# Optimization experiments

Measured on AMD Instinct MI355X. Metric: run time of the kernel, lower is better.

## Reference

```python
import jax, jax.numpy as jnp
import numpy as np

CUTOFF = 4.0
RBF_N = 32          # distance_embedding_size == D_rbf
F_DIM = 128         # hidden_size
N_ATOMS = 20000
N_PROBES = 100000
N_EDGES = 262144
LN_EPS = 1e-5


def setup_inputs() -> dict:
    key = jax.random.key(0)
    ks = jax.random.split(key, 20)
    s = 0.02
    inp = {
        "diff_pi": jax.random.normal(ks[0], (N_EDGES, 3), jnp.float32),
        "S_JK": jax.random.normal(ks[1], (N_ATOMS, F_DIM), jnp.float32),
        "V_JK": jax.random.normal(ks[2], (N_ATOMS, 3, F_DIM), jnp.float32),
        "atom_idx": jax.random.randint(ks[3], (N_EDGES,), 0, N_ATOMS),
        "probe_idx": jax.random.randint(ks[4], (N_EDGES,), 0, N_PROBES),
        "num_probes": N_PROBES,
        # state branch params
        "w_s1": jax.random.normal(ks[5], (3 * F_DIM, F_DIM), jnp.float32) * s,
        "b_s1": jnp.zeros((F_DIM,), jnp.float32),
        "g_ln": jnp.ones((F_DIM,), jnp.float32),
        "b_ln": jnp.zeros((F_DIM,), jnp.float32),
        "w_s2": jax.random.normal(ks[6], (F_DIM, F_DIM), jnp.float32) * s,
        "b_s2": jnp.zeros((F_DIM,), jnp.float32),
        # filter branch params
        "w_f1": jax.random.normal(ks[7], (RBF_N, F_DIM), jnp.float32) * s,
        "b_f1": jnp.zeros((F_DIM,), jnp.float32),
        "w_f2": jax.random.normal(ks[8], (F_DIM, F_DIM), jnp.float32) * s,
        "b_f2": jnp.zeros((F_DIM,), jnp.float32),
        # output head params
        "w_o1": jax.random.normal(ks[9], (F_DIM, F_DIM // 2), jnp.float32) * s,
        "b_o1": jnp.zeros((F_DIM // 2,), jnp.float32),
        "w_o2": jax.random.normal(ks[10], (F_DIM // 2, 1), jnp.float32) * s,
        "b_o2": jnp.zeros((1,), jnp.float32),
        "final_bias": jnp.array([-6.1], jnp.float32),
    }
    return inp


def reference(diff_pi, S_JK, V_JK, atom_idx, probe_idx, num_probes,
              w_s1, b_s1, g_ln, b_ln, w_s2, b_s2,
              w_f1, b_f1, w_f2, b_f2,
              w_o1, b_o1, w_o2, b_o2, final_bias):
    silu = jax.nn.silu
    # edge distances
    sq = (diff_pi ** 2).sum(-1)                       # [E]
    dist = jnp.sqrt(sq)                               # [E] exact distance
    dist_safe = jnp.sqrt(sq + 1e-8)[:, None]          # [E,1]
    r_hat = diff_pi / dist_safe                       # [E,3]

    # sinc RBF expansion: sin(n*pi*d/cutoff)/d, n=1..RBF_N
    n = jnp.arange(1, RBF_N + 1, dtype=diff_pi.dtype) # [D]
    e_pi = jnp.sin(dist[:, None] * n * (jnp.pi / CUTOFF)) / dist[:, None]  # [E,D]

    # gather atom features to edges
    n_i = jnp.sqrt((V_JK ** 2).sum(1) + 1e-8)         # [N,F]
    n_e = n_i[atom_idx]                               # [E,F]
    V_e = V_JK[atom_idx]                              # [E,3,F]
    q_pi = (V_e * r_hat[:, :, None]).sum(1)           # [E,F]
    S_e = S_JK[atom_idx]                              # [E,F]

    # state branch: Linear -> LayerNorm -> SiLU -> Linear
    h = jnp.concatenate([S_e, n_e, q_pi], axis=-1)    # [E,3F]
    u = h @ w_s1 + b_s1                               # [E,F]
    mu = u.mean(-1, keepdims=True)
    var = ((u - mu) ** 2).mean(-1, keepdims=True)
    u_norm = (u - mu) / jnp.sqrt(var + LN_EPS) * g_ln + b_ln
    state = silu(u_norm) @ w_s2 + b_s2                # [E,F]

    # filter branch (no normalization -> absolute distance scale)
    W = silu(e_pi @ w_f1 + b_f1) @ w_f2 + b_f2        # [E,F]

    # fuse + output head
    m = (silu((W * state) @ w_o1 + b_o1) @ w_o2 + b_o2)[:, 0]  # [E]

    x = dist / CUTOFF
    env = 1.0 - 21.0 * x ** 5 + 35.0 * x ** 6 - 15.0 * x ** 7
    env = jnp.where(dist < CUTOFF, env, jnp.zeros_like(env))
    m_w = m * env

    # scatter-add to probes
    rho = jax.ops.segment_sum(m_w, probe_idx, num_segments=num_probes)
    return rho + final_bias[0]
```

## Files before the change

kernel.cpp:

```cpp
#include <hip/hip_runtime.h>

#define EPB     64
#define E_TOTAL 262144
#define NPROBE  100000
#define N_ATOMS 20000

#define ASTR   136
#define A2_O   0
#define F1_O   8704
#define EPI_O  17408
#define DIST_O 19968
#define LDS_SH 20096

#define WS1_O  0
#define WS2_O  49152
#define WF1_O  65536
#define WF2_O  69632
#define WO1_O  86016
#define WT_TOT 94208
#define PQ_O   WT_TOT

typedef __attribute__((ext_vector_type(8))) short          short8;
typedef __attribute__((ext_vector_type(8))) unsigned short ushort8;
typedef __attribute__((ext_vector_type(4))) float          floatx4;

#define MFMA16(a, b, c) __builtin_amdgcn_mfma_f32_16x16x32_bf16((a), (b), (c), 0, 0, 0)

__device__ __forceinline__ short f2bf(float x) {
    unsigned u = __builtin_bit_cast(unsigned, x);
    u = (u + 0x7FFFu + ((u >> 16) & 1u)) >> 16;
    return (short)(unsigned short)u;
}
__device__ __forceinline__ unsigned pk2(float lo, float hi) {
    return __builtin_amdgcn_perm(__builtin_bit_cast(unsigned, hi),
                                 __builtin_bit_cast(unsigned, lo), 0x07060302u);
}
__device__ __forceinline__ float bf2f(unsigned short u) {
    return __builtin_bit_cast(float, ((unsigned)u) << 16);
}
__device__ __forceinline__ float silu_f(float x) {
    return x * __builtin_amdgcn_rcpf(1.0f + __expf(-x));
}

struct F8 { float v[8]; };
__device__ __forceinline__ F8 ld8(const float* __restrict__ p) {
    F8 r;
    const float4 a = *(const float4*)p;
    const float4 b = *(const float4*)(p + 4);
    r.v[0] = a.x; r.v[1] = a.y; r.v[2] = a.z; r.v[3] = a.w;
    r.v[4] = b.x; r.v[5] = b.y; r.v[6] = b.z; r.v[7] = b.w;
    return r;
}

__global__ void cfr_prep_w(const float* __restrict__ w_s1, const float* __restrict__ w_s2,
                           const float* __restrict__ w_f1, const float* __restrict__ w_f2,
                           const float* __restrict__ w_o1,
                           const float* __restrict__ fb, float* __restrict__ out,
                           unsigned short* __restrict__ wt) {
    int i = blockIdx.x * 256 + threadIdx.x;
    if (i < NPROBE) out[i] = fb[0];
    if (i < WT_TOT) {
        float v;
        if (i < WS2_O)      { int n = i / 384, k = i - n * 384;          v = w_s1[k * 128 + n]; }
        else if (i < WF1_O) { int j = i - WS2_O, n = j >> 7, k = j & 127; v = w_s2[k * 128 + n]; }
        else if (i < WF2_O) { int j = i - WF1_O, n = j >> 5, k = j & 31;  v = w_f1[k * 128 + n]; }
        else if (i < WO1_O) { int j = i - WF2_O, n = j >> 7, k = j & 127; v = w_f2[k * 128 + n]; }
        else                { int j = i - WO1_O, n = j >> 7, k = j & 127; v = w_o1[k * 64 + n]; }
        wt[i] = (unsigned short)f2bf(v);
    }
}

__global__ __launch_bounds__(256, 2) void cfr_prep_pq(
    const float* __restrict__ S, const float* __restrict__ V,
    const float* __restrict__ b_s1,
    const unsigned short* __restrict__ wt, unsigned short* __restrict__ pq)
{
    __shared__ __align__(16) unsigned short bufH[64 * 256];
    __shared__ __align__(16) unsigned short bufV[192 * 128];

    const int t    = threadIdx.x;
    const int a0   = blockIdx.x * 64;
    const int wave = t >> 6;
    const int lane = t & 63;
    const int q    = lane >> 4;
    const int c16  = lane & 15;

#pragma unroll
    for (int it = 0; it < 4; ++it) {
        int idx = it * 256 + t;
        int al = idx >> 4, f8 = (idx & 15) * 8;
        int a = a0 + al;
        ushort8 sS, sN, s0, s1, s2;
        if (a < N_ATOMS) {
            F8 s  = ld8(S + a * 128 + f8);
            F8 v0 = ld8(V + a * 384 + f8);
            F8 v1 = ld8(V + a * 384 + 128 + f8);
            F8 v2 = ld8(V + a * 384 + 256 + f8);
#pragma unroll
            for (int j = 0; j < 8; ++j) {
                sS[j] = (unsigned short)f2bf(s.v[j]);
                sN[j] = (unsigned short)f2bf(sqrtf(v0.v[j]*v0.v[j] + v1.v[j]*v1.v[j] + v2.v[j]*v2.v[j] + 1e-8f));
                s0[j] = (unsigned short)f2bf(v0.v[j]);
                s1[j] = (unsigned short)f2bf(v1.v[j]);
                s2[j] = (unsigned short)f2bf(v2.v[j]);
            }
        } else {
#pragma unroll
            for (int j = 0; j < 8; ++j) { sS[j]=0; sN[j]=0; s0[j]=0; s1[j]=0; s2[j]=0; }
        }
        const unsigned swH = (unsigned)((al & 7) << 4);
        char* hrow  = (char*)bufH + al * 512;
        char* vbase = (char*)bufV;
        *(ushort8*)(hrow + ((f8 * 2) ^ swH))         = sS;
        *(ushort8*)(hrow + ((256 + f8 * 2) ^ swH))   = sN;
        *(ushort8*)(vbase + al * 256         + ((f8 * 2) ^ swH)) = s0;
        *(ushort8*)(vbase + (64 + al) * 256  + ((f8 * 2) ^ swH)) = s1;
        *(ushort8*)(vbase + (128 + al) * 256 + ((f8 * 2) ^ swH)) = s2;
    }
    __syncthreads();

    const floatx4 zero4 = {0.f, 0.f, 0.f, 0.f};
    const unsigned swr = (unsigned)((c16 & 7) << 4);
    float bs1c[2];
#pragma unroll
    for (int ni = 0; ni < 2; ++ni) bs1c[ni] = b_s1[wave * 32 + ni * 16 + c16];

    {
        floatx4 pacc[4][2];
#pragma unroll
        for (int mi = 0; mi < 4; ++mi) { pacc[mi][0] = zero4; pacc[mi][1] = zero4; }
#pragma unroll
        for (int kk = 0; kk < 8; ++kk) {
            short8 bfr[2], af[4];
#pragma unroll
            for (int ni = 0; ni < 2; ++ni) {
                int n = wave * 32 + ni * 16 + c16;
                bfr[ni] = *(const short8*)&wt[WS1_O + n * 384 + kk * 32 + q * 8];
            }
#pragma unroll
            for (int mi = 0; mi < 4; ++mi) {
                int row = mi * 16 + c16;
                af[mi] = *(const short8*)((const char*)bufH + row * 512 + ((unsigned)(kk * 64 + q * 16) ^ swr));
            }
#pragma unroll
            for (int mi = 0; mi < 4; ++mi)
#pragma unroll
                for (int ni = 0; ni < 2; ++ni)
                    pacc[mi][ni] = MFMA16(af[mi], bfr[ni], pacc[mi][ni]);
        }
#pragma unroll
        for (int mi = 0; mi < 4; ++mi)
#pragma unroll
            for (int r = 0; r < 4; ++r) {
                int a = a0 + mi * 16 + q * 4 + r;
                if (a < N_ATOMS)
#pragma unroll
                    for (int ni = 0; ni < 2; ++ni) {
                        int col = wave * 32 + ni * 16 + c16;
                        pq[a * 512 + col] = (unsigned short)f2bf(pacc[mi][ni][r] + bs1c[ni]);
                    }
            }
    }

    short8 bq[4][2];
#pragma unroll
    for (int kk = 0; kk < 4; ++kk)
#pragma unroll
        for (int ni = 0; ni < 2; ++ni) {
            int n = wave * 32 + ni * 16 + c16;
            bq[kk][ni] = *(const short8*)&wt[WS1_O + n * 384 + 256 + kk * 32 + q * 8];
        }
#pragma unroll
    for (int d = 0; d < 3; ++d) {
        floatx4 qacc[4][2];
#pragma unroll
        for (int mi = 0; mi < 4; ++mi) { qacc[mi][0] = zero4; qacc[mi][1] = zero4; }
#pragma unroll
        for (int kk = 0; kk < 4; ++kk) {
            short8 af[4];
#pragma unroll
            for (int mi = 0; mi < 4; ++mi) {
                int row = d * 64 + mi * 16 + c16;
                af[mi] = *(const short8*)((const char*)bufV + row * 256 + ((unsigned)(kk * 64 + q * 16) ^ swr));
            }
#pragma unroll
            for (int mi = 0; mi < 4; ++mi)
#pragma unroll
                for (int ni = 0; ni < 2; ++ni)
                    qacc[mi][ni] = MFMA16(af[mi], bq[kk][ni], qacc[mi][ni]);
        }
#pragma unroll
        for (int mi = 0; mi < 4; ++mi)
#pragma unroll
            for (int r = 0; r < 4; ++r) {
                int a = a0 + mi * 16 + q * 4 + r;
                if (a < N_ATOMS)
#pragma unroll
                    for (int ni = 0; ni < 2; ++ni) {
                        int col = wave * 32 + ni * 16 + c16;
                        pq[a * 512 + (1 + d) * 128 + col] = (unsigned short)f2bf(qacc[mi][ni][r]);
                    }
            }
    }
}

__global__ __launch_bounds__(256, 2) void cfr_main(
    const float* __restrict__ diff,
    const int* __restrict__ atom_idx, const int* __restrict__ probe_idx,
    const unsigned short* __restrict__ wt, const unsigned short* __restrict__ pq,
    const float* __restrict__ g_ln, const float* __restrict__ b_ln,
    const float* __restrict__ b_s2, const float* __restrict__ b_f1,
    const float* __restrict__ b_f2, const float* __restrict__ b_o1,
    const float* __restrict__ w_o2, const float* __restrict__ b_o2,
    float* __restrict__ out)
{
    __shared__ __align__(16) unsigned short LDSu[LDS_SH];
    float* mpart = (float*)&LDSu[EPI_O];
    float* distL = (float*)&LDSu[DIST_O];

    const int t    = threadIdx.x;
    const int e0   = blockIdx.x * EPB;
    const int wave = t >> 6;
    const int lane = t & 63;
    const int q    = lane >> 4;
    const int c16  = lane & 15;
    const floatx4 zero4 = {0.f, 0.f, 0.f, 0.f};

    short8 wbe[2];
    short8 wb2[4][2], wbw[4][2];
    short8 wbo[4];
    float  bf1c[2], bs2c[2], bf2c[2];
#pragma unroll
    for (int ni = 0; ni < 2; ++ni) {
        const int n = wave * 32 + ni * 16 + c16;
        wbe[ni] = *(const short8*)&wt[WF1_O + n * 32 + q * 8];
#pragma unroll
        for (int kk = 0; kk < 4; ++kk) {
            wb2[kk][ni] = *(const short8*)&wt[WS2_O + n * 128 + kk * 32 + q * 8];
            wbw[kk][ni] = *(const short8*)&wt[WF2_O + n * 128 + kk * 32 + q * 8];
        }
        bf1c[ni] = b_f1[n]; bs2c[ni] = b_s2[n]; bf2c[ni] = b_f2[n];
    }
    const int n2 = wave * 16 + c16;
#pragma unroll
    for (int kk = 0; kk < 4; ++kk)
        wbo[kk] = *(const short8*)&wt[WO1_O + n2 * 128 + kk * 32 + q * 8];
    const float bo1c = b_o1[n2], wo2c = w_o2[n2];

    {
        const int el = t >> 2;
        const int cc = t & 3;
        const int c0 = cc * 32;
        const int eg = e0 + el;
        const int a  = atom_idx[eg];
        float dx = diff[eg * 3 + 0], dy = diff[eg * 3 + 1], dz = diff[eg * 3 + 2];
        float sq   = dx * dx + dy * dy + dz * dz;
        float dist = sqrtf(sq);
        float rinv = rsqrtf(sq + 1e-8f);
        float rx = dx * rinv, ry = dy * rinv, rz = dz * rinv;
        if (cc == 0) distL[el] = dist;

        const ushort8* pqr = (const ushort8*)(pq + a * 512 + c0);
        float u[32];
#pragma unroll
        for (int g = 0; g < 4; ++g) {
            ushort8 v = pqr[g];
#pragma unroll
            for (int j = 0; j < 8; ++j) u[g * 8 + j] = bf2f(v[j]);
        }
#pragma unroll
        for (int g = 0; g < 4; ++g) {
            ushort8 v = pqr[16 + g];
#pragma unroll
            for (int j = 0; j < 8; ++j) u[g * 8 + j] = fmaf(bf2f(v[j]), rx, u[g * 8 + j]);
        }
#pragma unroll
        for (int g = 0; g < 4; ++g) {
            ushort8 v = pqr[32 + g];
#pragma unroll
            for (int j = 0; j < 8; ++j) u[g * 8 + j] = fmaf(bf2f(v[j]), ry, u[g * 8 + j]);
        }
#pragma unroll
        for (int g = 0; g < 4; ++g) {
            ushort8 v = pqr[48 + g];
#pragma unroll
            for (int j = 0; j < 8; ++j) u[g * 8 + j] = fmaf(bf2f(v[j]), rz, u[g * 8 + j]);
        }
        float s = 0.f, s2 = 0.f;
#pragma unroll
        for (int j = 0; j < 32; ++j) { s += u[j]; s2 = fmaf(u[j], u[j], s2); }
        s  += __shfl_xor(s, 1);  s  += __shfl_xor(s, 2);
        s2 += __shfl_xor(s2, 1); s2 += __shfl_xor(s2, 2);
        float mu = s * (1.f / 128.f);
        float rstd = rsqrtf(s2 * (1.f / 128.f) - mu * mu + 1e-5f);
        const float4* gp = (const float4*)(g_ln + c0);
        const float4* bp = (const float4*)(b_ln + c0);
        unsigned pko[16];
#pragma unroll
        for (int g4 = 0; g4 < 8; ++g4) {
            float4 gg = gp[g4], bb = bp[g4];
            float y0 = silu_f((u[g4 * 4 + 0] - mu) * rstd * gg.x + bb.x);
            float y1 = silu_f((u[g4 * 4 + 1] - mu) * rstd * gg.y + bb.y);
            float y2 = silu_f((u[g4 * 4 + 2] - mu) * rstd * gg.z + bb.z);
            float y3 = silu_f((u[g4 * 4 + 3] - mu) * rstd * gg.w + bb.w);
            pko[g4 * 2 + 0] = pk2(y0, y1);
            pko[g4 * 2 + 1] = pk2(y2, y3);
        }
        uint4* dst = (uint4*)&LDSu[A2_O + el * ASTR + c0];
        dst[0] = make_uint4(pko[0], pko[1], pko[2], pko[3]);
        dst[1] = make_uint4(pko[4], pko[5], pko[6], pko[7]);
        dst[2] = make_uint4(pko[8], pko[9], pko[10], pko[11]);
        dst[3] = make_uint4(pko[12], pko[13], pko[14], pko[15]);
        float inv = __builtin_amdgcn_rcpf(dist);
        float d8  = dist * 0.125f;
        float sv[8];
#pragma unroll
        for (int j = 0; j < 8; ++j) {
            float nf = (float)(cc * 8 + j + 1);
            sv[j] = __builtin_amdgcn_sinf(d8 * nf) * inv;
        }
        *(uint4*)&LDSu[EPI_O + el * 40 + cc * 8] =
            make_uint4(pk2(sv[0], sv[1]), pk2(sv[2], sv[3]), pk2(sv[4], sv[5]), pk2(sv[6], sv[7]));
    }
    __syncthreads();

    {
        short8 ae[4];
#pragma unroll
        for (int mi = 0; mi < 4; ++mi)
            ae[mi] = *(const short8*)&LDSu[EPI_O + (mi * 16 + c16) * 40 + q * 8];
        floatx4 facc[4][2];
#pragma unroll
        for (int mi = 0; mi < 4; ++mi)
#pragma unroll
            for (int ni = 0; ni < 2; ++ni)
                facc[mi][ni] = MFMA16(ae[mi], wbe[ni], zero4);
#pragma unroll
        for (int mi = 0; mi < 4; ++mi)
#pragma unroll
            for (int r = 0; r < 4; ++r) {
                int row = mi * 16 + q * 4 + r;
#pragma unroll
                for (int ni = 0; ni < 2; ++ni) {
                    float v = facc[mi][ni][r] + bf1c[ni];
                    LDSu[F1_O + row * ASTR + (wave * 32 + ni * 16 + c16)] =
                        (unsigned short)(__builtin_bit_cast(unsigned, silu_f(v)) >> 16);
                }
            }
    }
    __syncthreads();

    {
        floatx4 sacc[4][2], wacc[4][2];
#pragma unroll
        for (int mi = 0; mi < 4; ++mi)
#pragma unroll
            for (int ni = 0; ni < 2; ++ni) { sacc[mi][ni] = zero4; wacc[mi][ni] = zero4; }
#pragma unroll
        for (int kk = 0; kk < 4; ++kk) {
            short8 a2f[4], f1f[4];
#pragma unroll
            for (int mi = 0; mi < 4; ++mi) {
                a2f[mi] = *(const short8*)&LDSu[A2_O + (mi * 16 + c16) * ASTR + kk * 32 + q * 8];
                f1f[mi] = *(const short8*)&LDSu[F1_O + (mi * 16 + c16) * ASTR + kk * 32 + q * 8];
            }
#pragma unroll
            for (int mi = 0; mi < 4; ++mi)
#pragma unroll
                for (int ni = 0; ni < 2; ++ni) {
                    sacc[mi][ni] = MFMA16(a2f[mi], wb2[kk][ni], sacc[mi][ni]);
                    wacc[mi][ni] = MFMA16(f1f[mi], wbw[kk][ni], wacc[mi][ni]);
                }
        }
        __syncthreads();
#pragma unroll
        for (int mi = 0; mi < 4; ++mi)
#pragma unroll
            for (int r = 0; r < 4; ++r) {
                int row = mi * 16 + q * 4 + r;
#pragma unroll
                for (int ni = 0; ni < 2; ++ni) {
                    float g = (sacc[mi][ni][r] + bs2c[ni]) * (wacc[mi][ni][r] + bf2c[ni]);
                    LDSu[A2_O + row * ASTR + (wave * 32 + ni * 16 + c16)] =
                        (unsigned short)(__builtin_bit_cast(unsigned, g) >> 16);
                }
            }
    }
    __syncthreads();

    {
        floatx4 oacc[4];
#pragma unroll
        for (int mi = 0; mi < 4; ++mi) oacc[mi] = zero4;
#pragma unroll
        for (int kk = 0; kk < 4; ++kk) {
#pragma unroll
            for (int mi = 0; mi < 4; ++mi) {
                short8 af = *(const short8*)&LDSu[A2_O + (mi * 16 + c16) * ASTR + kk * 32 + q * 8];
                oacc[mi] = MFMA16(af, wbo[kk], oacc[mi]);
            }
        }
#pragma unroll
        for (int mi = 0; mi < 4; ++mi)
#pragma unroll
            for (int r = 0; r < 4; ++r) {
                float s = silu_f(oacc[mi][r] + bo1c) * wo2c;
#pragma unroll
                for (int d = 1; d < 16; d <<= 1) s += __shfl_xor(s, d, 64);
                if (c16 == 0) mpart[(mi * 16 + q * 4 + r) * 4 + wave] = s;
            }
    }
    __syncthreads();

    if (t < EPB) {
        int eg = e0 + t;
        float m = mpart[t * 4 + 0] + mpart[t * 4 + 1] + mpart[t * 4 + 2] + mpart[t * 4 + 3] + b_o2[0];
        float dist = distL[t];
        float x  = dist * 0.25f;
        float x2 = x * x, x4 = x2 * x2;
        float x5 = x4 * x, x6 = x5 * x, x7 = x6 * x;
        float env = 1.0f - 21.0f * x5 + 35.0f * x6 - 15.0f * x7;
        env = (dist < 4.0f) ? env : 0.0f;
        float mw = m * env;
        if (mw != 0.f) unsafeAtomicAdd(&out[probe_idx[eg]], mw);
    }
}

extern "C" void kernel_launch(void* const* d_in, const int* in_sizes, int n_in,
                              void* d_out, int out_size, void* d_ws, size_t ws_size,
                              hipStream_t stream) {
    const float* diff    = (const float*)d_in[0];
    const float* S_JK    = (const float*)d_in[1];
    const float* V_JK    = (const float*)d_in[2];
    const int*   atom_i  = (const int*)d_in[3];
    const int*   probe_i = (const int*)d_in[4];
    const float* w_s1 = (const float*)d_in[6];
    const float* b_s1 = (const float*)d_in[7];
    const float* g_ln = (const float*)d_in[8];
    const float* b_ln = (const float*)d_in[9];
    const float* w_s2 = (const float*)d_in[10];
    const float* b_s2 = (const float*)d_in[11];
    const float* w_f1 = (const float*)d_in[12];
    const float* b_f1 = (const float*)d_in[13];
    const float* w_f2 = (const float*)d_in[14];
    const float* b_f2 = (const float*)d_in[15];
    const float* w_o1 = (const float*)d_in[16];
    const float* b_o1 = (const float*)d_in[17];
    const float* w_o2 = (const float*)d_in[18];
    const float* b_o2 = (const float*)d_in[19];
    const float* fbias = (const float*)d_in[20];
    float* out = (float*)d_out;

    unsigned short* wt = (unsigned short*)d_ws;
    unsigned short* pqp = wt + PQ_O;

    cfr_prep_w<<<(NPROBE + 255) / 256, 256, 0, stream>>>(w_s1, w_s2, w_f1, w_f2, w_o1,
                                                         fbias, out, wt);
    cfr_prep_pq<<<(N_ATOMS + 63) / 64, 256, 0, stream>>>(S_JK, V_JK, b_s1, wt, pqp);
    cfr_main<<<E_TOTAL / EPB, 256, 0, stream>>>(diff, atom_i, probe_i, wt, pqp,
        g_ln, b_ln, b_s2, b_f1, b_f2, b_o1, w_o2, b_o2, out);
}
```

Baseline: 253.3 us.

## Give each wave its own 16-edge row slice and drop block barriers

Work is split by rows instead of by output columns: each wave owns 16 edges and computes all 128 output columns for them. That removes the __syncthreads between the filter, state and output stages, and the cross-wave partial-sum reduction through LDS. Weights are no longer held in registers; they are reloaded from global/L1 inside the MFMA loops. Launch bounds are raised so more blocks fit per CU. The change relies on each wave's first-phase LDS writes (rows el = t>>2 for its own threads) matching the rows it later reads, and it adds weight-fetch traffic in the inner loops.

```diff
diff --git a/kernel.cpp b/kernel.cpp
--- a/kernel.cpp
+++ b/kernel.cpp
@@ -204,7 +204,7 @@
     }
 }
 
-__global__ __launch_bounds__(256, 2) void cfr_main(
+__global__ __launch_bounds__(256, 4) void cfr_main(
     const float* __restrict__ diff,
     const int* __restrict__ atom_idx, const int* __restrict__ probe_idx,
     const unsigned short* __restrict__ wt, const unsigned short* __restrict__ pq,
@@ -215,7 +215,6 @@
     float* __restrict__ out)
 {
     __shared__ __align__(16) unsigned short LDSu[LDS_SH];
-    float* mpart = (float*)&LDSu[EPI_O];
     float* distL = (float*)&LDSu[DIST_O];
 
     const int t    = threadIdx.x;
@@ -225,27 +224,6 @@
     const int q    = lane >> 4;
     const int c16  = lane & 15;
     const floatx4 zero4 = {0.f, 0.f, 0.f, 0.f};
-
-    short8 wbe[2];
-    short8 wb2[4][2], wbw[4][2];
-    short8 wbo[4];
-    float  bf1c[2], bs2c[2], bf2c[2];
-#pragma unroll
-    for (int ni = 0; ni < 2; ++ni) {
-        const int n = wave * 32 + ni * 16 + c16;
-        wbe[ni] = *(const short8*)&wt[WF1_O + n * 32 + q * 8];
-#pragma unroll
-        for (int kk = 0; kk < 4; ++kk) {
-            wb2[kk][ni] = *(const short8*)&wt[WS2_O + n * 128 + kk * 32 + q * 8];
-            wbw[kk][ni] = *(const short8*)&wt[WF2_O + n * 128 + kk * 32 + q * 8];
-        }
-        bf1c[ni] = b_f1[n]; bs2c[ni] = b_s2[n]; bf2c[ni] = b_f2[n];
-    }
-    const int n2 = wave * 16 + c16;
-#pragma unroll
-    for (int kk = 0; kk < 4; ++kk)
-        wbo[kk] = *(const short8*)&wt[WO1_O + n2 * 128 + kk * 32 + q * 8];
-    const float bo1c = b_o1[n2], wo2c = w_o2[n2];
 
     {
         const int el = t >> 2;
@@ -322,107 +300,108 @@
         *(uint4*)&LDSu[EPI_O + el * 40 + cc * 8] =
             make_uint4(pk2(sv[0], sv[1]), pk2(sv[2], sv[3]), pk2(sv[4], sv[5]), pk2(sv[6], sv[7]));
     }
-    __syncthreads();
+
+    const int rbase = wave * 16;
 
     {
-        short8 ae[4];
-#pragma unroll
-        for (int mi = 0; mi < 4; ++mi)
-            ae[mi] = *(const short8*)&LDSu[EPI_O + (mi * 16 + c16) * 40 + q * 8];
-        floatx4 facc[4][2];
-#pragma unroll
-        for (int mi = 0; mi < 4; ++mi)
-#pragma unroll
-            for (int ni = 0; ni < 2; ++ni)
-                facc[mi][ni] = MFMA16(ae[mi], wbe[ni], zero4);
-#pragma unroll
-        for (int mi = 0; mi < 4; ++mi)
+        short8 ae = *(const short8*)&LDSu[EPI_O + (rbase + c16) * 40 + q * 8];
+        floatx4 facc[8];
+#pragma unroll
+        for (int ni = 0; ni < 8; ++ni) {
+            short8 be = *(const short8*)&wt[WF1_O + (ni * 16 + c16) * 32 + q * 8];
+            facc[ni] = MFMA16(ae, be, zero4);
+        }
+#pragma unroll
+        for (int ni = 0; ni < 8; ++ni) {
+            float bf1c = b_f1[ni * 16 + c16];
 #pragma unroll
             for (int r = 0; r < 4; ++r) {
-                int row = mi * 16 + q * 4 + r;
-#pragma unroll
-                for (int ni = 0; ni < 2; ++ni) {
-                    float v = facc[mi][ni][r] + bf1c[ni];
-                    LDSu[F1_O + row * ASTR + (wave * 32 + ni * 16 + c16)] =
-                        (unsigned short)(__builtin_bit_cast(unsigned, silu_f(v)) >> 16);
-                }
-            }
-    }
-    __syncthreads();
-
-    {
-        floatx4 sacc[4][2], wacc[4][2];
-#pragma unroll
-        for (int mi = 0; mi < 4; ++mi)
-#pragma unroll
-            for (int ni = 0; ni < 2; ++ni) { sacc[mi][ni] = zero4; wacc[mi][ni] = zero4; }
+                int row = rbase + q * 4 + r;
+                LDSu[F1_O + row * ASTR + ni * 16 + c16] =
+                    (unsigned short)(__builtin_bit_cast(unsigned, silu_f(facc[ni][r] + bf1c)) >> 16);
+            }
+        }
+    }
+
+    short8 aA[4], aF[4];
+#pragma unroll
+    for (int kk = 0; kk < 4; ++kk) {
+        aA[kk] = *(const short8*)&LDSu[A2_O + (rbase + c16) * ASTR + kk * 32 + q * 8];
+        aF[kk] = *(const short8*)&LDSu[F1_O + (rbase + c16) * ASTR + kk * 32 + q * 8];
+    }
+
+#pragma unroll
+    for (int h = 0; h < 2; ++h) {
+        floatx4 sacc[4], wacc[4];
+#pragma unroll
+        for (int ni = 0; ni < 4; ++ni) { sacc[ni] = zero4; wacc[ni] = zero4; }
 #pragma unroll
         for (int kk = 0; kk < 4; ++kk) {
-            short8 a2f[4], f1f[4];
-#pragma unroll
-            for (int mi = 0; mi < 4; ++mi) {
-                a2f[mi] = *(const short8*)&LDSu[A2_O + (mi * 16 + c16) * ASTR + kk * 32 + q * 8];
-                f1f[mi] = *(const short8*)&LDSu[F1_O + (mi * 16 + c16) * ASTR + kk * 32 + q * 8];
-            }
-#pragma unroll
-            for (int mi = 0; mi < 4; ++mi)
-#pragma unroll
-                for (int ni = 0; ni < 2; ++ni) {
-                    sacc[mi][ni] = MFMA16(a2f[mi], wb2[kk][ni], sacc[mi][ni]);
-                    wacc[mi][ni] = MFMA16(f1f[mi], wbw[kk][ni], wacc[mi][ni]);
-                }
-        }
-        __syncthreads();
-#pragma unroll
-        for (int mi = 0; mi < 4; ++mi)
+#pragma unroll
+            for (int ni = 0; ni < 4; ++ni) {
+                int n = h * 64 + ni * 16 + c16;
+                short8 b2 = *(const short8*)&wt[WS2_O + n * 128 + kk * 32 + q * 8];
+                short8 bw = *(const short8*)&wt[WF2_O + n * 128 + kk * 32 + q * 8];
+                sacc[ni] = MFMA16(aA[kk], b2, sacc[ni]);
+                wacc[ni] = MFMA16(aF[kk], bw, wacc[ni]);
+            }
+        }
+#pragma unroll
+        for (int ni = 0; ni < 4; ++ni) {
+            int col = h * 64 + ni * 16 + c16;
+            float bs2c = b_s2[col], bf2c = b_f2[col];
 #pragma unroll
             for (int r = 0; r < 4; ++r) {
-                int row = mi * 16 + q * 4 + r;
-#pragma unroll
-                for (int ni = 0; ni < 2; ++ni) {
-                    float g = (sacc[mi][ni][r] + bs2c[ni]) * (wacc[mi][ni][r] + bf2c[ni]);
-                    LDSu[A2_O + row * ASTR + (wave * 32 + ni * 16 + c16)] =
-                        (unsigned short)(__builtin_bit_cast(unsigned, g) >> 16);
-                }
-            }
-    }
-    __syncthreads();
+                int row = rbase + q * 4 + r;
+                float g = (sacc[ni][r] + bs2c) * (wacc[ni][r] + bf2c);
+                LDSu[A2_O + row * ASTR + col] =
+                    (unsigned short)(__builtin_bit_cast(unsigned, g) >> 16);
+            }
+        }
+    }
 
     {
         floatx4 oacc[4];
 #pragma unroll
-        for (int mi = 0; mi < 4; ++mi) oacc[mi] = zero4;
+        for (int ni = 0; ni < 4; ++ni) oacc[ni] = zero4;
 #pragma unroll
         for (int kk = 0; kk < 4; ++kk) {
-#pragma unroll
-            for (int mi = 0; mi < 4; ++mi) {
-                short8 af = *(const short8*)&LDSu[A2_O + (mi * 16 + c16) * ASTR + kk * 32 + q * 8];
-                oacc[mi] = MFMA16(af, wbo[kk], oacc[mi]);
-            }
-        }
-#pragma unroll
-        for (int mi = 0; mi < 4; ++mi)
-#pragma unroll
-            for (int r = 0; r < 4; ++r) {
-                float s = silu_f(oacc[mi][r] + bo1c) * wo2c;
-#pragma unroll
-                for (int d = 1; d < 16; d <<= 1) s += __shfl_xor(s, d, 64);
-                if (c16 == 0) mpart[(mi * 16 + q * 4 + r) * 4 + wave] = s;
-            }
-    }
-    __syncthreads();
-
-    if (t < EPB) {
-        int eg = e0 + t;
-        float m = mpart[t * 4 + 0] + mpart[t * 4 + 1] + mpart[t * 4 + 2] + mpart[t * 4 + 3] + b_o2[0];
-        float dist = distL[t];
-        float x  = dist * 0.25f;
-        float x2 = x * x, x4 = x2 * x2;
-        float x5 = x4 * x, x6 = x5 * x, x7 = x6 * x;
-        float env = 1.0f - 21.0f * x5 + 35.0f * x6 - 15.0f * x7;
-        env = (dist < 4.0f) ? env : 0.0f;
-        float mw = m * env;
-        if (mw != 0.f) unsafeAtomicAdd(&out[probe_idx[eg]], mw);
+            short8 af = *(const short8*)&LDSu[A2_O + (rbase + c16) * ASTR + kk * 32 + q * 8];
+#pragma unroll
+            for (int ni = 0; ni < 4; ++ni) {
+                short8 bo = *(const short8*)&wt[WO1_O + (ni * 16 + c16) * 128 + kk * 32 + q * 8];
+                oacc[ni] = MFMA16(af, bo, oacc[ni]);
+            }
+        }
+        float bo1c[4], wo2c[4];
+#pragma unroll
+        for (int ni = 0; ni < 4; ++ni) {
+            bo1c[ni] = b_o1[ni * 16 + c16];
+            wo2c[ni] = w_o2[ni * 16 + c16];
+        }
+        const float bo2v = b_o2[0];
+#pragma unroll
+        for (int r = 0; r < 4; ++r) {
+            float s = silu_f(oacc[0][r] + bo1c[0]) * wo2c[0]
+                    + silu_f(oacc[1][r] + bo1c[1]) * wo2c[1]
+                    + silu_f(oacc[2][r] + bo1c[2]) * wo2c[2]
+                    + silu_f(oacc[3][r] + bo1c[3]) * wo2c[3];
+#pragma unroll
+            for (int d = 1; d < 16; d <<= 1) s += __shfl_xor(s, d, 64);
+            if (c16 == 0) {
+                int el = rbase + q * 4 + r;
+                int eg = e0 + el;
+                float m = s + bo2v;
+                float dist = distL[el];
+                float x  = dist * 0.25f;
+                float x2 = x * x, x4 = x2 * x2;
+                float x5 = x4 * x, x6 = x5 * x, x7 = x6 * x;
+                float env = 1.0f - 21.0f * x5 + 35.0f * x6 - 15.0f * x7;
+                env = (dist < 4.0f) ? env : 0.0f;
+                float mw = m * env;
+                if (mw != 0.f) unsafeAtomicAdd(&out[probe_idx[eg]], mw);
+            }
+        }
     }
 }
 
```

Result: slower. 365.1 us (+44.1%).
